# Kernel tuning notes

Hardware: AMD Instinct MI355X
Metric: run time of the kernel (lower is better)

The kernel has to match this reference:

```python
import jax, jax.numpy as jnp
import numpy as np

B, T, F, H = 2048, 256, 128, 64


def setup_inputs() -> dict:
    key = jax.random.key(0)
    ks = jax.random.split(key, 7)
    s_ih = 1.0 / np.sqrt(H)
    return {
        "x": jax.random.normal(ks[0], (B, T, F), dtype=jnp.float32),
        "w_ih": jax.random.uniform(ks[1], (3 * H, F), jnp.float32, -s_ih, s_ih),
        "w_hh": jax.random.uniform(ks[2], (3 * H, H), jnp.float32, -s_ih, s_ih),
        "b_ih": jax.random.uniform(ks[3], (3 * H,), jnp.float32, -s_ih, s_ih),
        "b_hh": jax.random.uniform(ks[4], (3 * H,), jnp.float32, -s_ih, s_ih),
        "fc_w": jax.random.uniform(ks[5], (1, H), jnp.float32, -s_ih, s_ih),
        "fc_b": jax.random.uniform(ks[6], (1,), jnp.float32, -s_ih, s_ih),
    }


def _gru_last_hidden(x, w_ih, w_hh, b_ih, b_hh):
    # Precompute input projections for all timesteps: [B,T,3H] -> scan over T
    gx = jnp.einsum("btf,gf->btg", x, w_ih) + b_ih  # g = 3H
    gx = jnp.transpose(gx, (1, 0, 2))  # [T, B, 3H]
    h0 = jnp.zeros((x.shape[0], w_hh.shape[1]), dtype=x.dtype)
    Hd = w_hh.shape[1]

    def step(h, gx_t):
        gh = h @ w_hh.T + b_hh  # [B, 3H]
        rx, zx, nx = gx_t[:, :Hd], gx_t[:, Hd:2 * Hd], gx_t[:, 2 * Hd:]
        rh, zh, nh = gh[:, :Hd], gh[:, Hd:2 * Hd], gh[:, 2 * Hd:]
        r = jax.nn.sigmoid(rx + rh)
        z = jax.nn.sigmoid(zx + zh)
        n = jnp.tanh(nx + r * nh)
        h_new = (1.0 - z) * n + z * h
        return h_new, None

    h_last, _ = jax.lax.scan(step, h0, gx)
    return h_last  # [B, H]


def reference(x, w_ih, w_hh, b_ih, b_hh, fc_w, fc_b):
    # eval mode: dropout is identity
    h_last = _gru_last_hidden(x, w_ih, w_hh, b_ih, b_hh)
    return h_last @ fc_w.T + fc_b  # [B, 1]
```

## Files before the change

### kernel.cpp

```cpp
#include <hip/hip_runtime.h>
#include <math.h>

#define B_ 2048
#define T_ 256
#define F_ 128
#define H_ 64
#define G_ 192
#define TC_ 16
#define NCH_ (T_ / TC_)
#define NW_ 8
#define GXS 193

typedef __attribute__((ext_vector_type(8))) short short8;
typedef __attribute__((ext_vector_type(4))) float f32x4;

__device__ __forceinline__ unsigned short bf16_rne(float f) {
    unsigned int u = __float_as_uint(f);
    u += 0x7fffu + ((u >> 16) & 1u);
    return (unsigned short)(u >> 16);
}
__device__ __forceinline__ float bf16_to_f32(unsigned short h) {
    return __uint_as_float(((unsigned int)h) << 16);
}
__device__ __forceinline__ float sigmoid_f(float v) { return 1.0f / (1.0f + __expf(-v)); }
__device__ __forceinline__ float tanh_f(float v) {
    return 1.0f - 2.0f / (1.0f + __expf(2.0f * v));
}

__global__ __launch_bounds__(512, 2) void gru_fused(
    const float* __restrict__ x, const float* __restrict__ w_ih,
    const float* __restrict__ w_hh, const float* __restrict__ b_ih,
    const float* __restrict__ b_hh, const float* __restrict__ fc_w,
    const float* __restrict__ fc_b, float* __restrict__ out)
{
    __shared__ short sh_wfrag[12 * 4 * 64 * 8];
    __shared__ float sh_gxl[NW_ * TC_ * GXS];
    __shared__ float sh_bias[G_];
    __shared__ float sh_h[NW_][H_];

    const int tid = threadIdx.x;
    const int wv  = tid >> 6;
    const int j   = tid & 63;
    const int brow = blockIdx.x * NW_ + wv;

    for (int s = tid; s < 12 * 4 * 64; s += 512) {
        const int n = s >> 8;
        const int r = s & 255;
        const int ks = r >> 6;
        const int L = r & 63;
        const int g = n * 16 + (L & 15);
        const int k0 = ks * 32 + (L >> 4) * 8;
        const float4 w0 = *(const float4*)&w_ih[g * F_ + k0];
        const float4 w1 = *(const float4*)&w_ih[g * F_ + k0 + 4];
        union { short8 v; unsigned short u[8]; } fr;
        fr.u[0] = bf16_rne(w0.x); fr.u[1] = bf16_rne(w0.y);
        fr.u[2] = bf16_rne(w0.z); fr.u[3] = bf16_rne(w0.w);
        fr.u[4] = bf16_rne(w1.x); fr.u[5] = bf16_rne(w1.y);
        fr.u[6] = bf16_rne(w1.z); fr.u[7] = bf16_rne(w1.w);
        *(short8*)&sh_wfrag[s * 8] = fr.v;
    }
    for (int i = tid; i < G_; i += 512) sh_bias[i] = b_ih[i];

    float4 wr[16], wz[16], wn[16];
    #pragma unroll
    for (int k4 = 0; k4 < 16; ++k4) {
        wr[k4] = *(const float4*)&w_hh[(j)       * H_ + k4 * 4];
        wz[k4] = *(const float4*)&w_hh[(64 + j)  * H_ + k4 * 4];
        wn[k4] = *(const float4*)&w_hh[(128 + j) * H_ + k4 * 4];
    }
    const float bR = b_hh[j], bZ = b_hh[64 + j], bN = b_hh[128 + j];

    float* gxw = &sh_gxl[wv * TC_ * GXS];
    float* hw  = sh_h[wv];
    float hval = 0.0f;
    hw[j] = 0.0f;

    __syncthreads();

    for (int c = 0; c < NCH_; ++c) {
        const int t0 = c * TC_;

        const float* xb = x + ((size_t)brow * T_ + t0 + (j & 15)) * F_ + ((j >> 4) * 8);
        short8 ah[4], al[4];
        #pragma unroll
        for (int ks = 0; ks < 4; ++ks) {
            const float4 a0 = *(const float4*)(xb + ks * 32);
            const float4 a1 = *(const float4*)(xb + ks * 32 + 4);
            const float f[8] = {a0.x, a0.y, a0.z, a0.w, a1.x, a1.y, a1.z, a1.w};
            union { short8 v; unsigned short u[8]; } Hi, Lo;
            #pragma unroll
            for (int e = 0; e < 8; ++e) {
                const unsigned short hb = bf16_rne(f[e]);
                Hi.u[e] = hb;
                Lo.u[e] = bf16_rne(f[e] - bf16_to_f32(hb));
            }
            ah[ks] = Hi.v; al[ks] = Lo.v;
        }

        #pragma unroll
        for (int n = 0; n < 12; ++n) {
            const float bv = sh_bias[n * 16 + (j & 15)];
            f32x4 acc = {bv, bv, bv, bv};
            #pragma unroll
            for (int ks = 0; ks < 4; ++ks) {
                const short8 wf = *(const short8*)&sh_wfrag[((n * 4 + ks) * 64 + j) * 8];
                acc = __builtin_amdgcn_mfma_f32_16x16x32_bf16(ah[ks], wf, acc, 0, 0, 0);
                acc = __builtin_amdgcn_mfma_f32_16x16x32_bf16(al[ks], wf, acc, 0, 0, 0);
            }
            const int colb = n * 16 + (j & 15);
            const int s0 = (j >> 4) * 4;
            gxw[(s0 + 0) * GXS + colb] = acc[0];
            gxw[(s0 + 1) * GXS + colb] = acc[1];
            gxw[(s0 + 2) * GXS + colb] = acc[2];
            gxw[(s0 + 3) * GXS + colb] = acc[3];
        }

        for (int tt = 0; tt < TC_; ++tt) {
            const float rx = gxw[tt * GXS + j];
            const float zx = gxw[tt * GXS + 64 + j];
            const float nx = gxw[tt * GXS + 128 + j];

            float aR = bR, aZ = bZ, aN = bN;
            #pragma unroll
            for (int k4 = 0; k4 < 16; ++k4) {
                const float4 h4 = *(const float4*)&hw[k4 * 4];
                aR = fmaf(wr[k4].x, h4.x, aR); aR = fmaf(wr[k4].y, h4.y, aR);
                aR = fmaf(wr[k4].z, h4.z, aR); aR = fmaf(wr[k4].w, h4.w, aR);
                aZ = fmaf(wz[k4].x, h4.x, aZ); aZ = fmaf(wz[k4].y, h4.y, aZ);
                aZ = fmaf(wz[k4].z, h4.z, aZ); aZ = fmaf(wz[k4].w, h4.w, aZ);
                aN = fmaf(wn[k4].x, h4.x, aN); aN = fmaf(wn[k4].y, h4.y, aN);
                aN = fmaf(wn[k4].z, h4.z, aN); aN = fmaf(wn[k4].w, h4.w, aN);
            }
            const float r = sigmoid_f(rx + aR);
            const float z = sigmoid_f(zx + aZ);
            const float n = tanh_f(nx + r * aN);
            hval = (1.0f - z) * n + z * hval;
            hw[j] = hval;
            __builtin_amdgcn_wave_barrier();
        }
    }

    float v = hval * fc_w[j];
    #pragma unroll
    for (int m = 32; m >= 1; m >>= 1) v += __shfl_xor(v, m, 64);
    if (j == 0) out[brow] = v + fc_b[0];
}

extern "C" void kernel_launch(void* const* d_in, const int* in_sizes, int n_in,
                              void* d_out, int out_size, void* d_ws, size_t ws_size,
                              hipStream_t stream)
{
    (void)in_sizes; (void)n_in; (void)out_size; (void)d_ws; (void)ws_size;
    const float* x    = (const float*)d_in[0];
    const float* w_ih = (const float*)d_in[1];
    const float* w_hh = (const float*)d_in[2];
    const float* b_ih = (const float*)d_in[3];
    const float* b_hh = (const float*)d_in[4];
    const float* fc_w = (const float*)d_in[5];
    const float* fc_b = (const float*)d_in[6];
    float* out = (float*)d_out;

    gru_fused<<<dim3(B_ / NW_), 512, 0, stream>>>(
        x, w_ih, w_hh, b_ih, b_hh, fc_w, fc_b, out);
}
```

Baseline: 680.4 us.

## Move recurrent h@W_hh onto MFMA with hi/lo bf16 split and 4-row blocks

Restructures the kernel so each 128-thread block handles 4 batch rows, and the recurrent matmul h@W_hh now runs on bf16 MFMA. The hidden state is split into high and low bf16 parts to keep precision. The input projection is now computed per timestep in MFMA, with x loads double-buffered in registers and prefetched ahead. The old per-chunk shared-memory gx buffer and the scalar FMA loops are gone. This adds a block-wide __syncthreads every timestep and uses 16-row MFMAs where only 4 rows are valid, wasting MFMA throughput. x is also rounded to bf16 with no low part, which reduces accuracy.

```diff
diff --git a/kernel.cpp b/kernel.cpp
--- a/kernel.cpp
+++ b/kernel.cpp
@@ -1,149 +1,238 @@
 #include <hip/hip_runtime.h>
-#include <math.h>
 
 #define B_ 2048
 #define T_ 256
 #define F_ 128
 #define H_ 64
-#define G_ 192
-#define TC_ 16
-#define NCH_ (T_ / TC_)
-#define NW_ 8
-#define GXS 193
 
 typedef __attribute__((ext_vector_type(8))) short short8;
 typedef __attribute__((ext_vector_type(4))) float f32x4;
 
-__device__ __forceinline__ unsigned short bf16_rne(float f) {
-    unsigned int u = __float_as_uint(f);
-    u += 0x7fffu + ((u >> 16) & 1u);
-    return (unsigned short)(u >> 16);
-}
-__device__ __forceinline__ float bf16_to_f32(unsigned short h) {
-    return __uint_as_float(((unsigned int)h) << 16);
-}
-__device__ __forceinline__ float sigmoid_f(float v) { return 1.0f / (1.0f + __expf(-v)); }
+__device__ __forceinline__ unsigned int rne2(float fa, float fb) {
+    unsigned int ua = __float_as_uint(fa);
+    unsigned int ub = __float_as_uint(fb);
+    ua = ua + 0x7fffu + ((ua >> 16) & 1u);
+    ub = ub + 0x7fffu + ((ub >> 16) & 1u);
+    return (ua >> 16) | (ub & 0xffff0000u);
+}
+__device__ __forceinline__ float sigmoid_f(float v) {
+    return __fdividef(1.0f, 1.0f + __expf(-v));
+}
 __device__ __forceinline__ float tanh_f(float v) {
-    return 1.0f - 2.0f / (1.0f + __expf(2.0f * v));
-}
-
-__global__ __launch_bounds__(512, 2) void gru_fused(
+    return 1.0f - __fdividef(2.0f, 1.0f + __expf(2.0f * v));
+}
+
+__global__ __launch_bounds__(128, 2) void gru_fused(
     const float* __restrict__ x, const float* __restrict__ w_ih,
     const float* __restrict__ w_hh, const float* __restrict__ b_ih,
     const float* __restrict__ b_hh, const float* __restrict__ fc_w,
     const float* __restrict__ fc_b, float* __restrict__ out)
 {
-    __shared__ short sh_wfrag[12 * 4 * 64 * 8];
-    __shared__ float sh_gxl[NW_ * TC_ * GXS];
-    __shared__ float sh_bias[G_];
-    __shared__ float sh_h[NW_][H_];
+    __shared__ __align__(16) short wihf[12 * 4 * 64 * 8];
+    __shared__ __align__(16) short whhf[12 * 2 * 64 * 8];
+    __shared__ __align__(16) short hhi_l[2][4][72];
+    __shared__ __align__(16) short hlo_l[2][4][72];
+    __shared__ float wred[2][4];
 
     const int tid = threadIdx.x;
     const int wv  = tid >> 6;
     const int j   = tid & 63;
-    const int brow = blockIdx.x * NW_ + wv;
-
-    for (int s = tid; s < 12 * 4 * 64; s += 512) {
-        const int n = s >> 8;
-        const int r = s & 255;
-        const int ks = r >> 6;
-        const int L = r & 63;
-        const int g = n * 16 + (L & 15);
-        const int k0 = ks * 32 + (L >> 4) * 8;
-        const float4 w0 = *(const float4*)&w_ih[g * F_ + k0];
-        const float4 w1 = *(const float4*)&w_ih[g * F_ + k0 + 4];
-        union { short8 v; unsigned short u[8]; } fr;
-        fr.u[0] = bf16_rne(w0.x); fr.u[1] = bf16_rne(w0.y);
-        fr.u[2] = bf16_rne(w0.z); fr.u[3] = bf16_rne(w0.w);
-        fr.u[4] = bf16_rne(w1.x); fr.u[5] = bf16_rne(w1.y);
-        fr.u[6] = bf16_rne(w1.z); fr.u[7] = bf16_rne(w1.w);
-        *(short8*)&sh_wfrag[s * 8] = fr.v;
-    }
-    for (int i = tid; i < G_; i += 512) sh_bias[i] = b_ih[i];
-
-    float4 wr[16], wz[16], wn[16];
+    const int q   = j >> 4;
+    const int c   = j & 15;
+    const int brow = blockIdx.x * 4;
+
+    for (int s = tid; s < 12 * 4 * 64; s += 128) {
+        const int n = s >> 8, ks = (s >> 6) & 3, L = s & 63;
+        const float* wp = w_ih + (n * 16 + (L & 15)) * F_ + ks * 32 + ((L >> 4) * 8);
+        const float4 a = *(const float4*)wp;
+        const float4 b = *(const float4*)(wp + 4);
+        union { short8 v; unsigned int u[4]; } fr;
+        fr.u[0] = rne2(a.x, a.y); fr.u[1] = rne2(a.z, a.w);
+        fr.u[2] = rne2(b.x, b.y); fr.u[3] = rne2(b.z, b.w);
+        *(short8*)&wihf[s * 8] = fr.v;
+    }
+    for (int s = tid; s < 12 * 2 * 64; s += 128) {
+        const int n = s >> 7, ks2 = (s >> 6) & 1, L = s & 63;
+        const float* wp = w_hh + (n * 16 + (L & 15)) * H_ + ks2 * 32 + ((L >> 4) * 8);
+        const float4 a = *(const float4*)wp;
+        const float4 b = *(const float4*)(wp + 4);
+        union { short8 v; unsigned int u[4]; } fr;
+        fr.u[0] = rne2(a.x, a.y); fr.u[1] = rne2(a.z, a.w);
+        fr.u[2] = rne2(b.x, b.y); fr.u[3] = rne2(b.z, b.w);
+        *(short8*)&whhf[s * 8] = fr.v;
+    }
+    for (int i = tid; i < 2 * 4 * 72; i += 128) {
+        ((short*)hhi_l)[i] = 0;
+        ((short*)hlo_l)[i] = 0;
+    }
+
+    const int d0 = wv * 32 + c;
+    float bxr[2], bxz[2], bxn[2], bgr[2], bgz[2], bgn[2];
     #pragma unroll
-    for (int k4 = 0; k4 < 16; ++k4) {
-        wr[k4] = *(const float4*)&w_hh[(j)       * H_ + k4 * 4];
-        wz[k4] = *(const float4*)&w_hh[(64 + j)  * H_ + k4 * 4];
-        wn[k4] = *(const float4*)&w_hh[(128 + j) * H_ + k4 * 4];
-    }
-    const float bR = b_hh[j], bZ = b_hh[64 + j], bN = b_hh[128 + j];
-
-    float* gxw = &sh_gxl[wv * TC_ * GXS];
-    float* hw  = sh_h[wv];
-    float hval = 0.0f;
-    hw[j] = 0.0f;
+    for (int n2 = 0; n2 < 2; ++n2) {
+        const int d = d0 + n2 * 16;
+        bxr[n2] = b_ih[d];        bgr[n2] = b_hh[d];
+        bxz[n2] = b_ih[64 + d];   bgz[n2] = b_hh[64 + d];
+        bxn[n2] = b_ih[128 + d];  bgn[n2] = b_hh[128 + d];
+    }
+    const float fw0 = fc_w[d0], fw1 = fc_w[d0 + 16];
+
+    const int xrow = (j & 15) & 3;
+    const int xsl  = (j & 15) >> 3;
+    const float* xlane = x + ((size_t)(brow + xrow) * T_ + xsl) * F_ + q * 8;
 
     __syncthreads();
 
-    for (int c = 0; c < NCH_; ++c) {
-        const int t0 = c * TC_;
-
-        const float* xb = x + ((size_t)brow * T_ + t0 + (j & 15)) * F_ + ((j >> 4) * 8);
-        short8 ah[4], al[4];
+    float4 XA[8], XB[8];
+    {
+        const float* lp = xlane;
         #pragma unroll
         for (int ks = 0; ks < 4; ++ks) {
-            const float4 a0 = *(const float4*)(xb + ks * 32);
-            const float4 a1 = *(const float4*)(xb + ks * 32 + 4);
-            const float f[8] = {a0.x, a0.y, a0.z, a0.w, a1.x, a1.y, a1.z, a1.w};
-            union { short8 v; unsigned short u[8]; } Hi, Lo;
-            #pragma unroll
-            for (int e = 0; e < 8; ++e) {
-                const unsigned short hb = bf16_rne(f[e]);
-                Hi.u[e] = hb;
-                Lo.u[e] = bf16_rne(f[e] - bf16_to_f32(hb));
-            }
-            ah[ks] = Hi.v; al[ks] = Lo.v;
-        }
-
-        #pragma unroll
-        for (int n = 0; n < 12; ++n) {
-            const float bv = sh_bias[n * 16 + (j & 15)];
-            f32x4 acc = {bv, bv, bv, bv};
+            XA[2 * ks]     = *(const float4*)(lp + ks * 32);
+            XA[2 * ks + 1] = *(const float4*)(lp + ks * 32 + 4);
+        }
+        lp = xlane + 2 * F_;
+        #pragma unroll
+        for (int ks = 0; ks < 4; ++ks) {
+            XB[2 * ks]     = *(const float4*)(lp + ks * 32);
+            XB[2 * ks + 1] = *(const float4*)(lp + ks * 32 + 4);
+        }
+    }
+
+    short8 af[4], hh[2], hl[2];
+    const short8 z8 = {0, 0, 0, 0, 0, 0, 0, 0};
+    hh[0] = z8; hh[1] = z8; hl[0] = z8; hl[1] = z8;
+
+    auto cvtbuf = [&](float4 (&Xv)[8]) {
+        #pragma unroll
+        for (int ks = 0; ks < 4; ++ks) {
+            union { short8 v; unsigned int u[4]; } fr;
+            fr.u[0] = rne2(Xv[2 * ks].x,     Xv[2 * ks].y);
+            fr.u[1] = rne2(Xv[2 * ks].z,     Xv[2 * ks].w);
+            fr.u[2] = rne2(Xv[2 * ks + 1].x, Xv[2 * ks + 1].y);
+            fr.u[3] = rne2(Xv[2 * ks + 1].z, Xv[2 * ks + 1].w);
+            af[ks] = fr.v;
+        }
+    };
+    cvtbuf(XA);
+
+    auto do_macro = [&](float4 (&Xre)[8], float4 (&Xcv)[8], int t0) {
+        f32x4 axr[2], axz[2], axn[2];
+        #pragma unroll
+        for (int n2 = 0; n2 < 2; ++n2) {
+            axr[n2] = (f32x4){bxr[n2], bxr[n2], bxr[n2], bxr[n2]};
+            axz[n2] = (f32x4){bxz[n2], bxz[n2], bxz[n2], bxz[n2]};
+            axn[n2] = (f32x4){bxn[n2], bxn[n2], bxn[n2], bxn[n2]};
+            const int tr = (0 + wv * 2 + n2) * 2048;
+            const int tz = (4 + wv * 2 + n2) * 2048;
+            const int tn = (8 + wv * 2 + n2) * 2048;
             #pragma unroll
             for (int ks = 0; ks < 4; ++ks) {
-                const short8 wf = *(const short8*)&sh_wfrag[((n * 4 + ks) * 64 + j) * 8];
-                acc = __builtin_amdgcn_mfma_f32_16x16x32_bf16(ah[ks], wf, acc, 0, 0, 0);
-                acc = __builtin_amdgcn_mfma_f32_16x16x32_bf16(al[ks], wf, acc, 0, 0, 0);
-            }
-            const int colb = n * 16 + (j & 15);
-            const int s0 = (j >> 4) * 4;
-            gxw[(s0 + 0) * GXS + colb] = acc[0];
-            gxw[(s0 + 1) * GXS + colb] = acc[1];
-            gxw[(s0 + 2) * GXS + colb] = acc[2];
-            gxw[(s0 + 3) * GXS + colb] = acc[3];
-        }
-
-        for (int tt = 0; tt < TC_; ++tt) {
-            const float rx = gxw[tt * GXS + j];
-            const float zx = gxw[tt * GXS + 64 + j];
-            const float nx = gxw[tt * GXS + 128 + j];
-
-            float aR = bR, aZ = bZ, aN = bN;
-            #pragma unroll
-            for (int k4 = 0; k4 < 16; ++k4) {
-                const float4 h4 = *(const float4*)&hw[k4 * 4];
-                aR = fmaf(wr[k4].x, h4.x, aR); aR = fmaf(wr[k4].y, h4.y, aR);
-                aR = fmaf(wr[k4].z, h4.z, aR); aR = fmaf(wr[k4].w, h4.w, aR);
-                aZ = fmaf(wz[k4].x, h4.x, aZ); aZ = fmaf(wz[k4].y, h4.y, aZ);
-                aZ = fmaf(wz[k4].z, h4.z, aZ); aZ = fmaf(wz[k4].w, h4.w, aZ);
-                aN = fmaf(wn[k4].x, h4.x, aN); aN = fmaf(wn[k4].y, h4.y, aN);
-                aN = fmaf(wn[k4].z, h4.z, aN); aN = fmaf(wn[k4].w, h4.w, aN);
-            }
-            const float r = sigmoid_f(rx + aR);
-            const float z = sigmoid_f(zx + aZ);
-            const float n = tanh_f(nx + r * aN);
-            hval = (1.0f - z) * n + z * hval;
-            hw[j] = hval;
-            __builtin_amdgcn_wave_barrier();
-        }
-    }
-
-    float v = hval * fc_w[j];
-    #pragma unroll
-    for (int m = 32; m >= 1; m >>= 1) v += __shfl_xor(v, m, 64);
-    if (j == 0) out[brow] = v + fc_b[0];
+                axr[n2] = __builtin_amdgcn_mfma_f32_16x16x32_bf16(
+                    af[ks], *(const short8*)&wihf[tr + ks * 512 + j * 8], axr[n2], 0, 0, 0);
+                axz[n2] = __builtin_amdgcn_mfma_f32_16x16x32_bf16(
+                    af[ks], *(const short8*)&wihf[tz + ks * 512 + j * 8], axz[n2], 0, 0, 0);
+                axn[n2] = __builtin_amdgcn_mfma_f32_16x16x32_bf16(
+                    af[ks], *(const short8*)&wihf[tn + ks * 512 + j * 8], axn[n2], 0, 0, 0);
+            }
+        }
+        {
+            int tl = t0 + 4; if (tl > 254) tl = 254;
+            const float* lp = xlane + (size_t)tl * F_;
+            #pragma unroll
+            for (int ks = 0; ks < 4; ++ks) {
+                Xre[2 * ks]     = *(const float4*)(lp + ks * 32);
+                Xre[2 * ks + 1] = *(const float4*)(lp + ks * 32 + 4);
+            }
+        }
+        auto step = [&](int s) {
+            f32x4 agr[2], agz[2], agn[2];
+            #pragma unroll
+            for (int n2 = 0; n2 < 2; ++n2) {
+                agr[n2] = (f32x4){bgr[n2], bgr[n2], bgr[n2], bgr[n2]};
+                agz[n2] = (f32x4){bgz[n2], bgz[n2], bgz[n2], bgz[n2]};
+                agn[n2] = (f32x4){bgn[n2], bgn[n2], bgn[n2], bgn[n2]};
+                const int tr = (0 + wv * 2 + n2) * 1024;
+                const int tz = (4 + wv * 2 + n2) * 1024;
+                const int tn = (8 + wv * 2 + n2) * 1024;
+                #pragma unroll
+                for (int ks2 = 0; ks2 < 2; ++ks2) {
+                    const short8 br = *(const short8*)&whhf[tr + ks2 * 512 + j * 8];
+                    const short8 bz = *(const short8*)&whhf[tz + ks2 * 512 + j * 8];
+                    const short8 bn = *(const short8*)&whhf[tn + ks2 * 512 + j * 8];
+                    agr[n2] = __builtin_amdgcn_mfma_f32_16x16x32_bf16(hh[ks2], br, agr[n2], 0, 0, 0);
+                    agr[n2] = __builtin_amdgcn_mfma_f32_16x16x32_bf16(hl[ks2], br, agr[n2], 0, 0, 0);
+                    agz[n2] = __builtin_amdgcn_mfma_f32_16x16x32_bf16(hh[ks2], bz, agz[n2], 0, 0, 0);
+                    agz[n2] = __builtin_amdgcn_mfma_f32_16x16x32_bf16(hl[ks2], bz, agz[n2], 0, 0, 0);
+                    agn[n2] = __builtin_amdgcn_mfma_f32_16x16x32_bf16(hh[ks2], bn, agn[n2], 0, 0, 0);
+                    agn[n2] = __builtin_amdgcn_mfma_f32_16x16x32_bf16(hl[ks2], bn, agn[n2], 0, 0, 0);
+                }
+            }
+            if ((q >> 1) == s) {
+                const int rowsel = q & 1;
+                #pragma unroll
+                for (int n2 = 0; n2 < 2; ++n2) {
+                    const int d = d0 + n2 * 16;
+                    #pragma unroll
+                    for (int rl = 0; rl < 2; ++rl) {
+                        const int row = rowsel * 2 + rl;
+                        const float vr  = rowsel ? axr[n2][2 + rl] + agr[n2][2 + rl]
+                                                 : axr[n2][rl]     + agr[n2][rl];
+                        const float vz  = rowsel ? axz[n2][2 + rl] + agz[n2][2 + rl]
+                                                 : axz[n2][rl]     + agz[n2][rl];
+                        const float vnx = rowsel ? axn[n2][2 + rl] : axn[n2][rl];
+                        const float vnh = rowsel ? agn[n2][2 + rl] : agn[n2][rl];
+                        const float r = sigmoid_f(vr);
+                        const float z = sigmoid_f(vz);
+                        const float n = tanh_f(vnx + r * vnh);
+                        const float hp =
+                            __uint_as_float(((unsigned int)(unsigned short)hhi_l[s][row][d]) << 16) +
+                            __uint_as_float(((unsigned int)(unsigned short)hlo_l[s][row][d]) << 16);
+                        const float hn = n + z * (hp - n);
+                        const unsigned int uh = __float_as_uint(hn);
+                        const unsigned int rr = uh + 0x7fffu + ((uh >> 16) & 1u);
+                        const float hif = __uint_as_float(rr & 0xffff0000u);
+                        const float lof = hn - hif;
+                        const unsigned int ul = __float_as_uint(lof);
+                        const unsigned int r2 = ul + 0x7fffu + ((ul >> 16) & 1u);
+                        hhi_l[s ^ 1][row][d] = (short)(rr >> 16);
+                        hlo_l[s ^ 1][row][d] = (short)(r2 >> 16);
+                    }
+                }
+            }
+            __syncthreads();
+            #pragma unroll
+            for (int ks2 = 0; ks2 < 2; ++ks2) {
+                hh[ks2] = *(const short8*)&hhi_l[s ^ 1][xrow][ks2 * 32 + q * 8];
+                hl[ks2] = *(const short8*)&hlo_l[s ^ 1][xrow][ks2 * 32 + q * 8];
+            }
+        };
+        step(0);
+        step(1);
+        cvtbuf(Xcv);
+    };
+
+    #pragma unroll 1
+    for (int t0 = 0; t0 < T_; t0 += 4) {
+        do_macro(XA, XB, t0);
+        do_macro(XB, XA, t0 + 2);
+    }
+
+    {
+        const int row = q;
+        const float hv0 =
+            __uint_as_float(((unsigned int)(unsigned short)hhi_l[0][row][d0]) << 16) +
+            __uint_as_float(((unsigned int)(unsigned short)hlo_l[0][row][d0]) << 16);
+        const float hv1 =
+            __uint_as_float(((unsigned int)(unsigned short)hhi_l[0][row][d0 + 16]) << 16) +
+            __uint_as_float(((unsigned int)(unsigned short)hlo_l[0][row][d0 + 16]) << 16);
+        float partial = hv0 * fw0 + hv1 * fw1;
+        #pragma unroll
+        for (int m = 1; m <= 8; m <<= 1) partial += __shfl_xor(partial, m, 64);
+        if (c == 0) wred[wv][q] = partial;
+        __syncthreads();
+        if (tid < 4) out[brow + tid] = wred[0][tid] + wred[1][tid] + fc_b[0];
+    }
 }
 
 extern "C" void kernel_launch(void* const* d_in, const int* in_sizes, int n_in,
@@ -160,6 +249,6 @@
     const float* fc_b = (const float*)d_in[6];
     float* out = (float*)d_out;
 
-    gru_fused<<<dim3(B_ / NW_), 512, 0, stream>>>(
+    gru_fused<<<dim3(B_ / 4), 128, 0, stream>>>(
         x, w_ih, w_hh, b_ih, b_hh, fc_w, fc_b, out);
 }
```

Result: faster. 631.2 us (-7.2%).
